# Optimization experiments

Measured on AMD Instinct MI355X. Metric: run time of the kernel, lower is better.

Reference implementation:

```python
import jax, jax.numpy as jnp
import numpy as np

B, T, C, H = 4, 2048, 1024, 16
HD = C // H  # head dim = 64


def setup_inputs() -> dict:
    key = jax.random.key(0)
    ks = jax.random.split(key, 5)
    s = 1.0 / np.sqrt(C)
    return {
        "x": jax.random.normal(ks[0], (B, T, C), jnp.float32),
        "Wk": jax.random.normal(ks[1], (C, C), jnp.float32) * s,
        "bk": jnp.zeros((C,), jnp.float32),
        "Wq": jax.random.normal(ks[2], (C, C), jnp.float32) * s,
        "bq": jnp.zeros((C,), jnp.float32),
        "Wv": jax.random.normal(ks[3], (C, C), jnp.float32) * s,
        "bv": jnp.zeros((C,), jnp.float32),
        "Wp": jax.random.normal(ks[4], (C, C), jnp.float32) * s,
        "bp": jnp.zeros((C,), jnp.float32),
    }


def reference(x, Wk, bk, Wq, bq, Wv, bv, Wp, bp):
    # Linear(in, out): y = x @ W.T + b  (W stored as [out, in], torch convention)
    k = (x @ Wk.T + bk).reshape(B, T, H, HD).transpose(0, 2, 1, 3)  # [B,H,T,HD]
    q = (x @ Wq.T + bq).reshape(B, T, H, HD).transpose(0, 2, 1, 3)
    v = (x @ Wv.T + bv).reshape(B, T, H, HD).transpose(0, 2, 1, 3)
    scale = 1.0 / np.sqrt(HD)
    att = jnp.einsum("bhqd,bhkd->bhqk", q, k) * scale  # [B,H,T,T]
    causal = jnp.tril(jnp.ones((T, T), bool))
    att = jnp.where(causal[None, None, :, :], att, -jnp.inf)
    att = jax.nn.softmax(att, axis=-1)
    y = jnp.einsum("bhqk,bhkd->bhqd", att, v)  # [B,H,T,HD]
    y = y.transpose(0, 2, 1, 3).reshape(B, T, C)
    return y @ Wp.T + bp
```

## Files before the change

kernel.cpp:

```cpp
#include <hip/hip_runtime.h>
#include <hip/hip_bf16.h>
#include <cmath>

#define Tt 2048
#define Cc 1024
#define Hh 16
#define HDd 64

typedef __attribute__((ext_vector_type(8))) short short8;
typedef __attribute__((ext_vector_type(4))) float f32x4;
typedef __attribute__((ext_vector_type(16))) float f32x16;

#define ASYNC16(gp, lp)                                       \
    __builtin_amdgcn_global_load_lds(                         \
        (const __attribute__((address_space(1))) void*)(gp),  \
        (__attribute__((address_space(3))) void*)(lp), 16, 0, 0)

__device__ __forceinline__ unsigned short f32_bf16(float f) {
    unsigned u = __float_as_uint(f);
    u += 0x7FFF + ((u >> 16) & 1);
    return (unsigned short)(u >> 16);
}
__device__ __forceinline__ unsigned short f32_bf16_rn(float f) {
    return (unsigned short)((__float_as_uint(f) + 0x8000u) >> 16);
}
__device__ __forceinline__ float fast_exp2(float x) {
#if __has_builtin(__builtin_amdgcn_exp2f)
    return __builtin_amdgcn_exp2f(x);
#else
    return exp2f(x);
#endif
}

__global__ __launch_bounds__(256) void cvt_all(
    const float* __restrict__ x, const float* __restrict__ a,
    const float* __restrict__ b, const float* __restrict__ c,
    const float* __restrict__ d, unsigned short* __restrict__ ox,
    unsigned short* __restrict__ oa, unsigned short* __restrict__ ob,
    unsigned short* __restrict__ oc, unsigned short* __restrict__ od) {
    const int id = blockIdx.x * 256 + threadIdx.x;
    const float* src; unsigned short* dst; int sub;
    if (id < 2097152) {
        src = x; dst = ox; sub = id;
    } else {
        const int wi = id - 2097152;
        const int which = wi >> 18;
        sub = wi & 262143;
        if (which == 0)      { src = a; dst = oa; }
        else if (which == 1) { src = b; dst = ob; }
        else if (which == 2) { src = c; dst = oc; }
        else                 { src = d; dst = od; }
    }
    float4 v = ((const float4*)src)[sub];
    ushort4 o;
    o.x = f32_bf16(v.x); o.y = f32_bf16(v.y);
    o.z = f32_bf16(v.z); o.w = f32_bf16(v.w);
    ((ushort4*)dst)[sub] = o;
}

__global__ __launch_bounds__(512, 2) void gemm_qkv8(
    const unsigned short* __restrict__ A,
    const unsigned short* __restrict__ Wcat,
    const float* __restrict__ bq, const float* __restrict__ bk,
    const float* __restrict__ bv,
    unsigned short* __restrict__ qout, unsigned short* __restrict__ kout,
    unsigned short* __restrict__ vout) {
    extern __shared__ unsigned short lds[];

    const int tid  = threadIdx.x;
    const int wid  = tid >> 6;
    const int lane = tid & 63;
    const int quad = lane >> 4;
    const int lr   = lane & 15;
    const int wr   = wid >> 2;
    const int wc   = wid & 3;

    const int id   = blockIdx.y * 8 + blockIdx.x;
    const int xcd  = id & 7;
    const int rank = id >> 3;
    const int by   = xcd * 4 + (rank >> 3);
    const int bx   = rank & 7;
    const int bm0  = by * 256;
    const int bn0  = bx * 256;

    const int srow  = wid * 8 + (lane >> 3);
    const int scol  = ((lane & 7) ^ (lane >> 3)) * 8;
    const int sldso = wid * 512;

    const int a_r   = wr * 64 + lr;
    const int b_r   = wc * 32 + lr;
    const int slot0 = (quad ^ (lr & 7)) * 8;
    const int slot1 = ((quad ^ 4) ^ (lr & 7)) * 8;

    f32x4 acc[8][4];
    const f32x4 zero = {0.f, 0.f, 0.f, 0.f};
#pragma unroll
    for (int i = 0; i < 8; ++i)
#pragma unroll
        for (int j = 0; j < 4; ++j) acc[i][j] = zero;

    short8 areg[4][2];
    short8 breg[2][2][2];

#define STG(S, BUF, REG, GB, GROW)                                          \
    do {                                                                    \
        if ((S) < 16) {                                                     \
            unsigned short* lb = lds + ((BUF) * 4 + (REG)) * 8192 + sldso;  \
            const unsigned short* gp =                                      \
                (GB) + (size_t)((GROW) + srow) * Cc + (S) * 64 + scol;      \
            ASYNC16(gp, lb);                                                \
            ASYNC16(gp + (size_t)64 * Cc, lb + 4096);                       \
        }                                                                   \
    } while (0)

#define LDA(mh)                                                             \
    do {                                                                    \
        const unsigned short* ab = bufb + (mh) * 8192;                      \
        _Pragma("unroll") for (int mf = 0; mf < 4; ++mf) {                  \
            areg[mf][0] = *(const short8*)(ab + (a_r + mf * 16) * 64 + slot0); \
            areg[mf][1] = *(const short8*)(ab + (a_r + mf * 16) * 64 + slot1); \
        }                                                                   \
    } while (0)

#define LDB(nh)                                                             \
    do {                                                                    \
        const unsigned short* bb = bufb + (2 + (nh)) * 8192;                \
        _Pragma("unroll") for (int nf = 0; nf < 2; ++nf) {                  \
            breg[nh][nf][0] = *(const short8*)(bb + (b_r + nf * 16) * 64 + slot0); \
            breg[nh][nf][1] = *(const short8*)(bb + (b_r + nf * 16) * 64 + slot1); \
        }                                                                   \
    } while (0)

#define MFMA_PHASE(mh, nh)                                                  \
    _Pragma("unroll") for (int mf = 0; mf < 4; ++mf)                        \
    _Pragma("unroll") for (int nf = 0; nf < 2; ++nf) {                      \
        acc[(mh)*4+mf][(nh)*2+nf] = __builtin_amdgcn_mfma_f32_16x16x32_bf16( \
            areg[mf][0], breg[nh][nf][0], acc[(mh)*4+mf][(nh)*2+nf], 0,0,0); \
        acc[(mh)*4+mf][(nh)*2+nf] = __builtin_amdgcn_mfma_f32_16x16x32_bf16( \
            areg[mf][1], breg[nh][nf][1], acc[(mh)*4+mf][(nh)*2+nf], 0,0,0); \
    }

#define TILE(T, BC, WN)                                                     \
    {                                                                       \
        const unsigned short* bufb = lds + (BC) * 32768;                    \
        LDA(0);                                                             \
        LDB(0);                                                             \
        STG((T) + 1, (BC) ^ 1, 1, A, bm0 + 128);                            \
        __builtin_amdgcn_s_barrier();                                       \
        asm volatile("s_waitcnt lgkmcnt(0)" ::: "memory");                  \
        __builtin_amdgcn_s_setprio(1);                                      \
        MFMA_PHASE(0, 0);                                                   \
        __builtin_amdgcn_s_setprio(0);                                      \
        __builtin_amdgcn_s_barrier();                                       \
        LDB(1);                                                             \
        STG((T) + 1, (BC) ^ 1, 3, Wcat, bn0 + 128);                         \
        __builtin_amdgcn_s_barrier();                                       \
        asm volatile("s_waitcnt lgkmcnt(0)" ::: "memory");                  \
        __builtin_amdgcn_s_setprio(1);                                      \
        MFMA_PHASE(0, 1);                                                   \
        __builtin_amdgcn_s_setprio(0);                                      \
        __builtin_amdgcn_s_barrier();                                       \
        LDA(1);                                                             \
        STG((T) + 2, (BC), 0, A, bm0);                                      \
        __builtin_amdgcn_s_barrier();                                       \
        asm volatile("s_waitcnt lgkmcnt(0)" ::: "memory");                  \
        __builtin_amdgcn_s_setprio(1);                                      \
        MFMA_PHASE(1, 0);                                                   \
        __builtin_amdgcn_s_setprio(0);                                      \
        __builtin_amdgcn_s_barrier();                                       \
        STG((T) + 2, (BC), 2, Wcat, bn0);                                   \
        __builtin_amdgcn_s_barrier();                                       \
        __builtin_amdgcn_s_setprio(1);                                      \
        MFMA_PHASE(1, 1);                                                   \
        __builtin_amdgcn_s_setprio(0);                                      \
        asm volatile("s_waitcnt vmcnt(" #WN ")" ::: "memory");              \
        __builtin_amdgcn_s_barrier();                                       \
    }

    STG(0, 0, 0, A, bm0);
    STG(0, 0, 1, A, bm0 + 128);
    STG(0, 0, 2, Wcat, bn0);
    STG(0, 0, 3, Wcat, bn0 + 128);
    STG(1, 1, 0, A, bm0);
    STG(1, 1, 2, Wcat, bn0);
    asm volatile("s_waitcnt vmcnt(4)" ::: "memory");
    __builtin_amdgcn_s_barrier();

    for (int t2 = 0; t2 < 7; ++t2) {
        const int T0 = t2 * 2;
        TILE(T0, 0, 4);
        TILE(T0 + 1, 1, 4);
    }
    TILE(14, 0, 0);
    TILE(15, 1, 0);

#undef TILE
#undef MFMA_PHASE
#undef LDB
#undef LDA
#undef STG

    const int which = bn0 >> 10;
    const float* bias = (which == 0) ? bq : bk;
    unsigned short* outp = (which == 0) ? qout : kout;
    const float scale = (which == 0) ? 0.1803368801111204f : 1.0f;
    const int nb = bn0 & 1023;
    (void)bv; (void)vout;

#pragma unroll
    for (int nh = 0; nh < 2; ++nh)
#pragma unroll
        for (int nf = 0; nf < 2; ++nf) {
            const int nl = nb + nh * 128 + wc * 32 + nf * 16 + lr;
            const float bvv = bias[nl];
            const int h = nl >> 6, hd = nl & 63;
#pragma unroll
            for (int mh = 0; mh < 2; ++mh)
#pragma unroll
                for (int mf = 0; mf < 4; ++mf) {
                    const f32x4 a = acc[mh * 4 + mf][nh * 2 + nf];
                    const int m0 = bm0 + mh * 128 + wr * 64 + mf * 16 + quad * 4;
                    const int b = m0 >> 11, t0 = m0 & 2047;
#pragma unroll
                    for (int r = 0; r < 4; ++r) {
                        outp[(((size_t)(b * Hh + h)) * Tt + t0 + r) * HDd + hd] =
                            f32_bf16_rn((a[r] + bvv) * scale);
                    }
                }
        }
}

__global__ __launch_bounds__(512, 2) void gemm_v8(
    const unsigned short* __restrict__ A,
    const unsigned short* __restrict__ Wcat,
    const float* __restrict__ bv,
    unsigned short* __restrict__ vout) {
    extern __shared__ unsigned short lds[];

    const int tid  = threadIdx.x;
    const int wid  = tid >> 6;
    const int lane = tid & 63;
    const int quad = lane >> 4;
    const int lr   = lane & 15;
    const int wr   = wid >> 2;
    const int wc   = wid & 3;

    const int id   = blockIdx.y * 8 + blockIdx.x;
    const int xcd  = id & 7;
    const int rank = id >> 3;
    const int by   = xcd * 4 + (rank >> 3);
    const int bx   = rank & 7;
    const int bm0  = by * 256;
    const int wrow0 = 2048 + bx * 128;

    const int srow  = wid * 8 + (lane >> 3);
    const int scol  = ((lane & 7) ^ (lane >> 3)) * 8;
    const int sldso = wid * 512;

    const int a_r   = wr * 64 + lr;
    const int b_r2  = (wc & 1) * 32 + lr;
    const int breg_off = 16384 + (wc >> 1) * 4096;
    const int slot0 = (quad ^ (lr & 7)) * 8;
    const int slot1 = ((quad ^ 4) ^ (lr & 7)) * 8;

    f32x4 acc[8][2];
    const f32x4 zero = {0.f, 0.f, 0.f, 0.f};
#pragma unroll
    for (int i = 0; i < 8; ++i)
#pragma unroll
        for (int j = 0; j < 2; ++j) acc[i][j] = zero;

    short8 areg[4][2];
    short8 breg[2][2];

#define STGAV(S, BUF, REG_OFF, GROW)                                        \
    do {                                                                    \
        if ((S) < 16) {                                                     \
            unsigned short* lb = lds + (BUF) * 24576 + (REG_OFF) + sldso;   \
            const unsigned short* gp =                                      \
                A + (size_t)(bm0 + (GROW) + srow) * Cc + (S) * 64 + scol;   \
            ASYNC16(gp, lb);                                                \
            ASYNC16(gp + (size_t)64 * Cc, lb + 4096);                       \
        }                                                                   \
    } while (0)

#define STGBV(S, BUF, REG_OFF, NROW)                                        \
    do {                                                                    \
        if ((S) < 16) {                                                     \
            unsigned short* lb = lds + (BUF) * 24576 + (REG_OFF) + sldso;   \
            const unsigned short* gp =                                      \
                Wcat + (size_t)(wrow0 + (NROW) + srow) * Cc + (S) * 64 + scol; \
            ASYNC16(gp, lb);                                                \
        }                                                                   \
    } while (0)

#define LDA_V(mh)                                                           \
    do {                                                                    \
        const unsigned short* ab = bufb + (mh) * 8192;                      \
        _Pragma("unroll") for (int mf = 0; mf < 4; ++mf) {                  \
            areg[mf][0] = *(const short8*)(ab + (a_r + mf * 16) * 64 + slot0); \
            areg[mf][1] = *(const short8*)(ab + (a_r + mf * 16) * 64 + slot1); \
        }                                                                   \
    } while (0)

#define LDB_V                                                               \
    do {                                                                    \
        const unsigned short* bb = bufb + breg_off;                         \
        _Pragma("unroll") for (int nf = 0; nf < 2; ++nf) {                  \
            breg[nf][0] = *(const short8*)(bb + (b_r2 + nf * 16) * 64 + slot0); \
            breg[nf][1] = *(const short8*)(bb + (b_r2 + nf * 16) * 64 + slot1); \
        }                                                                   \
    } while (0)

#define MFMA_V(mh)                                                          \
    _Pragma("unroll") for (int mf = 0; mf < 4; ++mf)                        \
    _Pragma("unroll") for (int nf = 0; nf < 2; ++nf) {                      \
        acc[(mh)*4+mf][nf] = __builtin_amdgcn_mfma_f32_16x16x32_bf16(       \
            areg[mf][0], breg[nf][0], acc[(mh)*4+mf][nf], 0, 0, 0);         \
        acc[(mh)*4+mf][nf] = __builtin_amdgcn_mfma_f32_16x16x32_bf16(       \
            areg[mf][1], breg[nf][1], acc[(mh)*4+mf][nf], 0, 0, 0);         \
    }

#define TILE_V(T, BC, WN)                                                   \
    {                                                                       \
        const unsigned short* bufb = lds + (BC) * 24576;                    \
        LDA_V(0);                                                           \
        LDB_V;                                                              \
        STGAV((T) + 1, (BC) ^ 1, 8192, 128);                                \
        STGBV((T) + 1, (BC) ^ 1, 20480, 64);                                \
        __builtin_amdgcn_s_barrier();                                       \
        asm volatile("s_waitcnt lgkmcnt(0)" ::: "memory");                  \
        __builtin_amdgcn_s_setprio(1);                                      \
        MFMA_V(0);                                                          \
        __builtin_amdgcn_s_setprio(0);                                      \
        __builtin_amdgcn_s_barrier();                                       \
        LDA_V(1);                                                           \
        STGAV((T) + 2, (BC), 0, 0);                                         \
        STGBV((T) + 2, (BC), 16384, 0);                                     \
        __builtin_amdgcn_s_barrier();                                       \
        asm volatile("s_waitcnt lgkmcnt(0)" ::: "memory");                  \
        __builtin_amdgcn_s_setprio(1);                                      \
        MFMA_V(1);                                                          \
        __builtin_amdgcn_s_setprio(0);                                      \
        asm volatile("s_waitcnt vmcnt(" #WN ")" ::: "memory");              \
        __builtin_amdgcn_s_barrier();                                       \
    }

    STGAV(0, 0, 0, 0);
    STGAV(0, 0, 8192, 128);
    STGBV(0, 0, 16384, 0);
    STGBV(0, 0, 20480, 64);
    STGAV(1, 1, 0, 0);
    STGBV(1, 1, 16384, 0);
    asm volatile("s_waitcnt vmcnt(3)" ::: "memory");
    __builtin_amdgcn_s_barrier();

    for (int t2 = 0; t2 < 7; ++t2) {
        const int T0 = t2 * 2;
        TILE_V(T0, 0, 3);
        TILE_V(T0 + 1, 1, 3);
    }
    TILE_V(14, 0, 0);
    TILE_V(15, 1, 0);

#undef TILE_V
#undef MFMA_V
#undef LDB_V
#undef LDA_V
#undef STGBV
#undef STGAV

#pragma unroll
    for (int nf = 0; nf < 2; ++nf) {
        const int nl = (wrow0 - 2048) + wc * 32 + nf * 16 + lr;
        const float bvv = bv[nl];
        const int h = nl >> 6, hd = nl & 63;
#pragma unroll
        for (int mh = 0; mh < 2; ++mh)
#pragma unroll
            for (int mf = 0; mf < 4; ++mf) {
                const f32x4 a = acc[mh * 4 + mf][nf];
                const int m0 = bm0 + mh * 128 + wr * 64 + mf * 16 + quad * 4;
                const int b = m0 >> 11, t0 = m0 & 2047;
                ushort4 pk;
                pk.x = f32_bf16_rn(a[0] + bvv);
                pk.y = f32_bf16_rn(a[1] + bvv);
                pk.z = f32_bf16_rn(a[2] + bvv);
                pk.w = f32_bf16_rn(a[3] + bvv);
                *(ushort4*)(vout + (((size_t)(b * Hh + h)) * HDd + hd) * Tt + t0) = pk;
            }
    }
}

__global__ __launch_bounds__(512, 2) void gemm_proj8(
    const unsigned short* __restrict__ A,
    const unsigned short* __restrict__ W,
    const float* __restrict__ bias,
    float* __restrict__ out) {
    extern __shared__ unsigned short lds[];

    const int tid  = threadIdx.x;
    const int wid  = tid >> 6;
    const int lane = tid & 63;
    const int quad = lane >> 4;
    const int lr   = lane & 15;
    const int wr   = wid >> 2;
    const int wc   = wid & 3;

    const int id   = blockIdx.y * 8 + blockIdx.x;
    const int xcd  = id & 7;
    const int rank = id >> 3;
    const int by   = xcd * 4 + (rank >> 3);
    const int bx   = rank & 7;
    const int bm0  = by * 256;
    const int bn0  = bx * 128;

    const int srow  = wid * 8 + (lane >> 3);
    const int scol  = ((lane & 7) ^ (lane >> 3)) * 8;
    const int sldso = wid * 512;

    const int a_r   = wr * 64 + lr;
    const int b_r2  = (wc & 1) * 32 + lr;
    const int breg_off = 16384 + (wc >> 1) * 4096;
    const int slot0 = (quad ^ (lr & 7)) * 8;
    const int slot1 = ((quad ^ 4) ^ (lr & 7)) * 8;

    f32x4 acc[8][2];
    const f32x4 zero = {0.f, 0.f, 0.f, 0.f};
#pragma unroll
    for (int i = 0; i < 8; ++i)
#pragma unroll
        for (int j = 0; j < 2; ++j) acc[i][j] = zero;

    short8 areg[4][2];
    short8 breg[2][2];

#define STGA(S, BUF, REG_OFF, GROW)                                         \
    do {                                                                    \
        if ((S) < 16) {                                                     \
            unsigned short* lb = lds + (BUF) * 24576 + (REG_OFF) + sldso;   \
            const unsigned short* gp =                                      \
                A + (size_t)(bm0 + (GROW) + srow) * Cc + (S) * 64 + scol;   \
            ASYNC16(gp, lb);                                                \
            ASYNC16(gp + (size_t)64 * Cc, lb + 4096);                       \
        }                                                                   \
    } while (0)

#define STGB(S, BUF, REG_OFF, NROW)                                         \
    do {                                                                    \
        if ((S) < 16) {                                                     \
            unsigned short* lb = lds + (BUF) * 24576 + (REG_OFF) + sldso;   \
            const unsigned short* gp =                                      \
                W + (size_t)(bn0 + (NROW) + srow) * Cc + (S) * 64 + scol;   \
            ASYNC16(gp, lb);                                                \
        }                                                                   \
    } while (0)

#define LDA_P(mh)                                                           \
    do {                                                                    \
        const unsigned short* ab = bufb + (mh) * 8192;                      \
        _Pragma("unroll") for (int mf = 0; mf < 4; ++mf) {                  \
            areg[mf][0] = *(const short8*)(ab + (a_r + mf * 16) * 64 + slot0); \
            areg[mf][1] = *(const short8*)(ab + (a_r + mf * 16) * 64 + slot1); \
        }                                                                   \
    } while (0)

#define LDB_P                                                               \
    do {                                                                    \
        const unsigned short* bb = bufb + breg_off;                         \
        _Pragma("unroll") for (int nf = 0; nf < 2; ++nf) {                  \
            breg[nf][0] = *(const short8*)(bb + (b_r2 + nf * 16) * 64 + slot0); \
            breg[nf][1] = *(const short8*)(bb + (b_r2 + nf * 16) * 64 + slot1); \
        }                                                                   \
    } while (0)

#define MFMA_P(mh)                                                          \
    _Pragma("unroll") for (int mf = 0; mf < 4; ++mf)                        \
    _Pragma("unroll") for (int nf = 0; nf < 2; ++nf) {                      \
        acc[(mh)*4+mf][nf] = __builtin_amdgcn_mfma_f32_16x16x32_bf16(       \
            areg[mf][0], breg[nf][0], acc[(mh)*4+mf][nf], 0, 0, 0);         \
        acc[(mh)*4+mf][nf] = __builtin_amdgcn_mfma_f32_16x16x32_bf16(       \
            areg[mf][1], breg[nf][1], acc[(mh)*4+mf][nf], 0, 0, 0);         \
    }

#define TILE_P(T, BC, WN)                                                   \
    {                                                                       \
        const unsigned short* bufb = lds + (BC) * 24576;                    \
        LDA_P(0);                                                           \
        LDB_P;                                                              \
        STGA((T) + 1, (BC) ^ 1, 8192, 128);                                 \
        STGB((T) + 1, (BC) ^ 1, 20480, 64);                                 \
        __builtin_amdgcn_s_barrier();                                       \
        asm volatile("s_waitcnt lgkmcnt(0)" ::: "memory");                  \
        __builtin_amdgcn_s_setprio(1);                                      \
        MFMA_P(0);                                                          \
        __builtin_amdgcn_s_setprio(0);                                      \
        __builtin_amdgcn_s_barrier();                                       \
        LDA_P(1);                                                           \
        STGA((T) + 2, (BC), 0, 0);                                          \
        STGB((T) + 2, (BC), 16384, 0);                                      \
        __builtin_amdgcn_s_barrier();                                       \
        asm volatile("s_waitcnt lgkmcnt(0)" ::: "memory");                  \
        __builtin_amdgcn_s_setprio(1);                                      \
        MFMA_P(1);                                                          \
        __builtin_amdgcn_s_setprio(0);                                      \
        asm volatile("s_waitcnt vmcnt(" #WN ")" ::: "memory");              \
        __builtin_amdgcn_s_barrier();                                       \
    }

    STGA(0, 0, 0, 0);
    STGA(0, 0, 8192, 128);
    STGB(0, 0, 16384, 0);
    STGB(0, 0, 20480, 64);
    STGA(1, 1, 0, 0);
    STGB(1, 1, 16384, 0);
    asm volatile("s_waitcnt vmcnt(3)" ::: "memory");
    __builtin_amdgcn_s_barrier();

    for (int t2 = 0; t2 < 7; ++t2) {
        const int T0 = t2 * 2;
        TILE_P(T0, 0, 3);
        TILE_P(T0 + 1, 1, 3);
    }
    TILE_P(14, 0, 0);
    TILE_P(15, 1, 0);

#undef TILE_P
#undef MFMA_P
#undef LDB_P
#undef LDA_P
#undef STGB
#undef STGA

#pragma unroll
    for (int nf = 0; nf < 2; ++nf) {
        const int n = bn0 + wc * 32 + nf * 16 + lr;
        const float bvv = bias[n];
#pragma unroll
        for (int mh = 0; mh < 2; ++mh)
#pragma unroll
            for (int mf = 0; mf < 4; ++mf) {
                const f32x4 a = acc[mh * 4 + mf][nf];
                const int m0 = bm0 + mh * 128 + wr * 64 + mf * 16 + quad * 4;
#pragma unroll
                for (int r = 0; r < 4; ++r)
                    out[(size_t)(m0 + r) * Cc + n] = a[r] + bvv;
            }
    }
}

__global__ __launch_bounds__(256, 2) void attn(const unsigned short* __restrict__ q,
                                               const unsigned short* __restrict__ k,
                                               const unsigned short* __restrict__ vt,
                                               unsigned short* __restrict__ y) {
    __shared__ unsigned short sK[2][64 * 64];
    __shared__ unsigned short sV[2][64 * 64];

    const int tid  = threadIdx.x;
    const int wid  = tid >> 6;
    const int lane = tid & 63;
    const int l31  = lane & 31;
    const int hb   = lane >> 5;
    const int x7   = lane & 7;

    const int bh = blockIdx.x;
    const int qx = blockIdx.y;
    const size_t headq = (size_t)bh * Tt * HDd;
    const unsigned short* kg = k + headq;
    const unsigned short* vg = vt + headq;
    const int b = bh >> 4, h = bh & 15;

    const int g_r = lane >> 3;
    const int g_c = ((lane & 7) ^ g_r) * 8;
    const unsigned short* kst = kg + (size_t)(wid * 16 + g_r) * HDd + g_c;
    const unsigned short* vst = vg + (size_t)(wid * 16 + g_r) * Tt + g_c;
    unsigned short* dK0 = sK[0] + wid * 1024;
    unsigned short* dK1 = sK[1] + wid * 1024;
    unsigned short* dV0 = sV[0] + wid * 1024;
    unsigned short* dV1 = sV[1] + wid * 1024;

#define STAGE_KV(BUF, KB)                                                   \
    do {                                                                    \
        unsigned short* dK = (BUF) ? dK1 : dK0;                             \
        unsigned short* dV = (BUF) ? dV1 : dV0;                             \
        ASYNC16(kst + (size_t)(KB) * HDd,       dK);                        \
        ASYNC16(kst + (size_t)((KB) + 8) * HDd, dK + 512);                  \
        ASYNC16(vst + (KB),                     dV);                        \
        ASYNC16(vst + (size_t)8 * Tt + (KB),    dV + 512);                  \
    } while (0)

#define CVTPK(d, a, bb) asm("v_cvt_pk_bf16_f32 %0, %1, %2" : "=v"(d) : "v"(a), "v"(bb))
#define PLSWAP(xx, yy)  asm("v_permlane32_swap_b32 %0, %1" : "+v"(xx), "+v"(yy))

    const int frow = l31 * 64;

    const f32x16 zero16 = {0.f,0.f,0.f,0.f,0.f,0.f,0.f,0.f,
                           0.f,0.f,0.f,0.f,0.f,0.f,0.f,0.f};

    const int nwoff = 1 + (wid >> 1);

    for (int pass = 0; pass < 2; ++pass) {
        const int qt = pass ? (15 - qx) : qx;
        const int qb = qt * 128;
        const int ntiles = 2 * qt + 2;
        const int nw = 2 * qt + nwoff;

        const unsigned short* qp =
            q + headq + (size_t)(qb + wid * 32 + l31) * HDd;
        short8 qf[4];
#pragma unroll
        for (int c = 0; c < 4; c++)
            qf[c] = *(const short8*)(qp + c * 16 + hb * 8);

        f32x16 o0 = zero16, o1 = zero16;
        float l_run = 0.f;

        STAGE_KV(0, 0);
        __syncthreads();

        for (int kt = 0; kt < ntiles; ++kt) {
            const int cur = kt & 1;
            if (kt + 1 < ntiles) STAGE_KV(cur ^ 1, (kt + 1) * 64);

            if (kt < nw) {
                const unsigned short* bK = sK[cur];
                const unsigned short* bV = sV[cur];

                f32x16 p0 = zero16, p1 = zero16;
                __builtin_amdgcn_s_setprio(1);
#pragma unroll
                for (int c = 0; c < 4; c++) {
                    const int cs = ((2 * c + hb) ^ x7) * 8;
                    short8 kf0 = *(const short8*)(bK + frow + cs);
                    short8 kf1 = *(const short8*)(bK + 2048 + frow + cs);
                    p0 = __builtin_amdgcn_mfma_f32_32x32x16_bf16(kf0, qf[c], p0, 0, 0, 0);
                    p1 = __builtin_amdgcn_mfma_f32_32x32x16_bf16(kf1, qf[c], p1, 0, 0, 0);
                }
                __builtin_amdgcn_s_setprio(0);

                if (kt == nw - 1 || kt == ntiles - 1) {
                    const int qd = qb + wid * 32 + l31 - kt * 64 - 4 * hb;
#pragma unroll
                    for (int r = 0; r < 16; r++) {
                        const int kb0 = (r & 3) + 8 * (r >> 2);
                        p0[r] = (kb0 <= qd) ? p0[r] : -INFINITY;
                        p1[r] = (kb0 + 32 <= qd) ? p1[r] : -INFINITY;
                    }
                }

                float lacc = 0.f;
#pragma unroll
                for (int r = 0; r < 16; r++) {
                    p0[r] = fast_exp2(p0[r]); lacc += p0[r];
                    p1[r] = fast_exp2(p1[r]); lacc += p1[r];
                }
                l_run += lacc;

                unsigned w0[4][2], w1[4][2];
#pragma unroll
                for (int g = 0; g < 4; g++) {
                    CVTPK(w0[g][0], p0[4 * g + 0], p0[4 * g + 1]);
                    CVTPK(w0[g][1], p0[4 * g + 2], p0[4 * g + 3]);
                    CVTPK(w1[g][0], p1[4 * g + 0], p1[4 * g + 1]);
                    CVTPK(w1[g][1], p1[4 * g + 2], p1[4 * g + 3]);
                }

                __builtin_amdgcn_s_setprio(1);
#pragma unroll
                for (int kc = 0; kc < 4; kc++) {
                    unsigned x0, x1, y0, y1;
                    if (kc == 0)      { x0 = w0[0][0]; x1 = w0[0][1]; y0 = w0[1][0]; y1 = w0[1][1]; }
                    else if (kc == 1) { x0 = w0[2][0]; x1 = w0[2][1]; y0 = w0[3][0]; y1 = w0[3][1]; }
                    else if (kc == 2) { x0 = w1[0][0]; x1 = w1[0][1]; y0 = w1[1][0]; y1 = w1[1][1]; }
                    else              { x0 = w1[2][0]; x1 = w1[2][1]; y0 = w1[3][0]; y1 = w1[3][1]; }
                    PLSWAP(x0, y0);
                    PLSWAP(x1, y1);
                    union { unsigned u[4]; short8 s; } pu;
                    pu.u[0] = x0; pu.u[1] = x1; pu.u[2] = y0; pu.u[3] = y1;

                    const int vs = ((2 * kc + hb) ^ x7) * 8;
                    short8 vf0 = *(const short8*)(bV + frow + vs);
                    short8 vf1 = *(const short8*)(bV + 2048 + frow + vs);
                    o0 = __builtin_amdgcn_mfma_f32_32x32x16_bf16(pu.s, vf0, o0, 0, 0, 0);
                    o1 = __builtin_amdgcn_mfma_f32_32x32x16_bf16(pu.s, vf1, o1, 0, 0, 0);
                }
                __builtin_amdgcn_s_setprio(0);
            }

            __syncthreads();
        }

        l_run += __shfl_xor(l_run, 32);
        const float inv = 1.0f / l_run;
        unsigned short* yp = y + (size_t)(b * Tt + qb + wid * 32) * Cc + h * HDd;
#pragma unroll
        for (int r = 0; r < 16; r++) {
            const int qr = (r & 3) + 8 * (r >> 2) + 4 * hb;
            const float invr = __shfl(inv, qr);
            yp[(size_t)qr * Cc + l31]      = f32_bf16_rn(o0[r] * invr);
            yp[(size_t)qr * Cc + 32 + l31] = f32_bf16_rn(o1[r] * invr);
        }
    }
#undef STAGE_KV
#undef CVTPK
#undef PLSWAP
}

extern "C" void kernel_launch(void* const* d_in, const int* in_sizes, int n_in,
                              void* d_out, int out_size, void* d_ws, size_t ws_size,
                              hipStream_t stream) {
    const float* x  = (const float*)d_in[0];
    const float* Wk = (const float*)d_in[1];
    const float* bk = (const float*)d_in[2];
    const float* Wq = (const float*)d_in[3];
    const float* bq = (const float*)d_in[4];
    const float* Wv = (const float*)d_in[5];
    const float* bv = (const float*)d_in[6];
    const float* Wp = (const float*)d_in[7];
    const float* bp = (const float*)d_in[8];
    float* out = (float*)d_out;

    char* ws = (char*)d_ws;
    size_t off = 0;
    auto alloc = [&](size_t bytes) { char* p = ws + off; off += bytes; return p; };
    const size_t MK = (size_t)8192 * 1024;
    const size_t NK = (size_t)1024 * 1024;
    unsigned short* xb   = (unsigned short*)alloc(MK * 2);
    unsigned short* Wcat = (unsigned short*)alloc(3 * NK * 2);
    unsigned short* Wqb  = Wcat;
    unsigned short* Wkb  = Wcat + NK;
    unsigned short* Wvb  = Wcat + 2 * NK;
    unsigned short* Wpb  = (unsigned short*)alloc(NK * 2);
    unsigned short* qh   = (unsigned short*)alloc(MK * 2);
    unsigned short* kh   = (unsigned short*)alloc(MK * 2);
    unsigned short* vth  = (unsigned short*)alloc(MK * 2);
    unsigned short* ya   = (unsigned short*)alloc(MK * 2);

    static bool lds_attr_set = false;
    if (!lds_attr_set) {
        (void)hipFuncSetAttribute((const void*)gemm_qkv8,
                                  hipFuncAttributeMaxDynamicSharedMemorySize,
                                  131072);
        (void)hipFuncSetAttribute((const void*)gemm_v8,
                                  hipFuncAttributeMaxDynamicSharedMemorySize,
                                  98304);
        (void)hipFuncSetAttribute((const void*)gemm_proj8,
                                  hipFuncAttributeMaxDynamicSharedMemorySize,
                                  98304);
        lds_attr_set = true;
    }

    cvt_all<<<12288, 256, 0, stream>>>(x, Wq, Wk, Wv, Wp, xb, Wqb, Wkb, Wvb, Wpb);

    gemm_qkv8<<<dim3(8, 32), 512, 131072, stream>>>(xb, Wcat, bq, bk, bv, qh, kh, vth);
    gemm_v8<<<dim3(8, 32), 512, 98304, stream>>>(xb, Wcat, bv, vth);

    attn<<<dim3(64, 8), 256, 0, stream>>>(qh, kh, vth, ya);

    gemm_proj8<<<dim3(8, 32), 512, 98304, stream>>>(ya, Wpb, bp, out);
}
```

Measured before the change: 229.2 us.

## Merge QK and V GEMMs into one launch and split attention into per-tile blocks

The separate QK and V projection kernels become one launch with 512 blocks that branch on block index, so one launch is saved and the two GEMMs can overlap. The attention kernel no longer loops over a paired short/long query tile in two passes. Each block now handles a single query tile from a 16-wide grid with a reordered tile mapping, and launch bounds are raised to 4 blocks per CU. This should improve occupancy and load balance but loses the explicit pairing, and the V part now reserves the larger 128 KB LDS allocation.

```diff
diff --git a/kernel.cpp b/kernel.cpp
--- a/kernel.cpp
+++ b/kernel.cpp
@@ -58,15 +58,12 @@
     ((ushort4*)dst)[sub] = o;
 }
 
-__global__ __launch_bounds__(512, 2) void gemm_qkv8(
+__device__ __forceinline__ void qk_body(
+    unsigned short* lds, const int id,
     const unsigned short* __restrict__ A,
     const unsigned short* __restrict__ Wcat,
     const float* __restrict__ bq, const float* __restrict__ bk,
-    const float* __restrict__ bv,
-    unsigned short* __restrict__ qout, unsigned short* __restrict__ kout,
-    unsigned short* __restrict__ vout) {
-    extern __shared__ unsigned short lds[];
-
+    unsigned short* __restrict__ qout, unsigned short* __restrict__ kout) {
     const int tid  = threadIdx.x;
     const int wid  = tid >> 6;
     const int lane = tid & 63;
@@ -75,7 +72,6 @@
     const int wr   = wid >> 2;
     const int wc   = wid & 3;
 
-    const int id   = blockIdx.y * 8 + blockIdx.x;
     const int xcd  = id & 7;
     const int rank = id >> 3;
     const int by   = xcd * 4 + (rank >> 3);
@@ -205,7 +201,6 @@
     unsigned short* outp = (which == 0) ? qout : kout;
     const float scale = (which == 0) ? 0.1803368801111204f : 1.0f;
     const int nb = bn0 & 1023;
-    (void)bv; (void)vout;
 
 #pragma unroll
     for (int nh = 0; nh < 2; ++nh)
@@ -230,13 +225,12 @@
         }
 }
 
-__global__ __launch_bounds__(512, 2) void gemm_v8(
+__device__ __forceinline__ void v_body(
+    unsigned short* lds, const int id,
     const unsigned short* __restrict__ A,
     const unsigned short* __restrict__ Wcat,
     const float* __restrict__ bv,
     unsigned short* __restrict__ vout) {
-    extern __shared__ unsigned short lds[];
-
     const int tid  = threadIdx.x;
     const int wid  = tid >> 6;
     const int lane = tid & 63;
@@ -245,7 +239,6 @@
     const int wr   = wid >> 2;
     const int wc   = wid & 3;
 
-    const int id   = blockIdx.y * 8 + blockIdx.x;
     const int xcd  = id & 7;
     const int rank = id >> 3;
     const int by   = xcd * 4 + (rank >> 3);
@@ -392,6 +385,21 @@
     }
 }
 
+__global__ __launch_bounds__(512, 2) void gemm_fused(
+    const unsigned short* __restrict__ A,
+    const unsigned short* __restrict__ Wcat,
+    const float* __restrict__ bq, const float* __restrict__ bk,
+    const float* __restrict__ bv,
+    unsigned short* __restrict__ qout, unsigned short* __restrict__ kout,
+    unsigned short* __restrict__ vout) {
+    extern __shared__ unsigned short lds[];
+    const int id = blockIdx.y * 8 + blockIdx.x;
+    if (id < 256)
+        qk_body(lds, id, A, Wcat, bq, bk, qout, kout);
+    else
+        v_body(lds, id - 256, A, Wcat, bv, vout);
+}
+
 __global__ __launch_bounds__(512, 2) void gemm_proj8(
     const unsigned short* __restrict__ A,
     const unsigned short* __restrict__ W,
@@ -549,7 +557,7 @@
     }
 }
 
-__global__ __launch_bounds__(256, 2) void attn(const unsigned short* __restrict__ q,
+__global__ __launch_bounds__(256, 4) void attn(const unsigned short* __restrict__ q,
                                                const unsigned short* __restrict__ k,
                                                const unsigned short* __restrict__ vt,
                                                unsigned short* __restrict__ y) {
@@ -564,7 +572,8 @@
     const int x7   = lane & 7;
 
     const int bh = blockIdx.x;
-    const int qx = blockIdx.y;
+    const int yb = blockIdx.y;
+    const int qt = (yb & 4) ? ((yb & 8) ? yb - 12 : yb + 4) : 15 - yb;
     const size_t headq = (size_t)bh * Tt * HDd;
     const unsigned short* kg = k + headq;
     const unsigned short* vg = vt + headq;
@@ -597,109 +606,104 @@
     const f32x16 zero16 = {0.f,0.f,0.f,0.f,0.f,0.f,0.f,0.f,
                            0.f,0.f,0.f,0.f,0.f,0.f,0.f,0.f};
 
-    const int nwoff = 1 + (wid >> 1);
-
-    for (int pass = 0; pass < 2; ++pass) {
-        const int qt = pass ? (15 - qx) : qx;
-        const int qb = qt * 128;
-        const int ntiles = 2 * qt + 2;
-        const int nw = 2 * qt + nwoff;
-
-        const unsigned short* qp =
-            q + headq + (size_t)(qb + wid * 32 + l31) * HDd;
-        short8 qf[4];
-#pragma unroll
-        for (int c = 0; c < 4; c++)
-            qf[c] = *(const short8*)(qp + c * 16 + hb * 8);
-
-        f32x16 o0 = zero16, o1 = zero16;
-        float l_run = 0.f;
-
-        STAGE_KV(0, 0);
+    const int qb = qt * 128;
+    const int ntiles = 2 * qt + 2;
+    const int nw = 2 * qt + 1 + (wid >> 1);
+
+    const unsigned short* qp =
+        q + headq + (size_t)(qb + wid * 32 + l31) * HDd;
+    short8 qf[4];
+#pragma unroll
+    for (int c = 0; c < 4; c++)
+        qf[c] = *(const short8*)(qp + c * 16 + hb * 8);
+
+    f32x16 o0 = zero16, o1 = zero16;
+    float l_run = 0.f;
+
+    STAGE_KV(0, 0);
+    __syncthreads();
+
+    for (int kt = 0; kt < ntiles; ++kt) {
+        const int cur = kt & 1;
+        if (kt + 1 < ntiles) STAGE_KV(cur ^ 1, (kt + 1) * 64);
+
+        if (kt < nw) {
+            const unsigned short* bK = sK[cur];
+            const unsigned short* bV = sV[cur];
+
+            f32x16 p0 = zero16, p1 = zero16;
+            __builtin_amdgcn_s_setprio(1);
+#pragma unroll
+            for (int c = 0; c < 4; c++) {
+                const int cs = ((2 * c + hb) ^ x7) * 8;
+                short8 kf0 = *(const short8*)(bK + frow + cs);
+                short8 kf1 = *(const short8*)(bK + 2048 + frow + cs);
+                p0 = __builtin_amdgcn_mfma_f32_32x32x16_bf16(kf0, qf[c], p0, 0, 0, 0);
+                p1 = __builtin_amdgcn_mfma_f32_32x32x16_bf16(kf1, qf[c], p1, 0, 0, 0);
+            }
+            __builtin_amdgcn_s_setprio(0);
+
+            if (kt == nw - 1 || kt == ntiles - 1) {
+                const int qd = qb + wid * 32 + l31 - kt * 64 - 4 * hb;
+#pragma unroll
+                for (int r = 0; r < 16; r++) {
+                    const int kb0 = (r & 3) + 8 * (r >> 2);
+                    p0[r] = (kb0 <= qd) ? p0[r] : -INFINITY;
+                    p1[r] = (kb0 + 32 <= qd) ? p1[r] : -INFINITY;
+                }
+            }
+
+            float lacc = 0.f;
+#pragma unroll
+            for (int r = 0; r < 16; r++) {
+                p0[r] = fast_exp2(p0[r]); lacc += p0[r];
+                p1[r] = fast_exp2(p1[r]); lacc += p1[r];
+            }
+            l_run += lacc;
+
+            unsigned w0[4][2], w1[4][2];
+#pragma unroll
+            for (int g = 0; g < 4; g++) {
+                CVTPK(w0[g][0], p0[4 * g + 0], p0[4 * g + 1]);
+                CVTPK(w0[g][1], p0[4 * g + 2], p0[4 * g + 3]);
+                CVTPK(w1[g][0], p1[4 * g + 0], p1[4 * g + 1]);
+                CVTPK(w1[g][1], p1[4 * g + 2], p1[4 * g + 3]);
+            }
+
+            __builtin_amdgcn_s_setprio(1);
+#pragma unroll
+            for (int kc = 0; kc < 4; kc++) {
+                unsigned x0, x1, y0, y1;
+                if (kc == 0)      { x0 = w0[0][0]; x1 = w0[0][1]; y0 = w0[1][0]; y1 = w0[1][1]; }
+                else if (kc == 1) { x0 = w0[2][0]; x1 = w0[2][1]; y0 = w0[3][0]; y1 = w0[3][1]; }
+                else if (kc == 2) { x0 = w1[0][0]; x1 = w1[0][1]; y0 = w1[1][0]; y1 = w1[1][1]; }
+                else              { x0 = w1[2][0]; x1 = w1[2][1]; y0 = w1[3][0]; y1 = w1[3][1]; }
+                PLSWAP(x0, y0);
+                PLSWAP(x1, y1);
+                union { unsigned u[4]; short8 s; } pu;
+                pu.u[0] = x0; pu.u[1] = x1; pu.u[2] = y0; pu.u[3] = y1;
+
+                const int vs = ((2 * kc + hb) ^ x7) * 8;
+                short8 vf0 = *(const short8*)(bV + frow + vs);
+                short8 vf1 = *(const short8*)(bV + 2048 + frow + vs);
+                o0 = __builtin_amdgcn_mfma_f32_32x32x16_bf16(pu.s, vf0, o0, 0, 0, 0);
+                o1 = __builtin_amdgcn_mfma_f32_32x32x16_bf16(pu.s, vf1, o1, 0, 0, 0);
+            }
+            __builtin_amdgcn_s_setprio(0);
+        }
+
         __syncthreads();
-
-        for (int kt = 0; kt < ntiles; ++kt) {
-            const int cur = kt & 1;
-            if (kt + 1 < ntiles) STAGE_KV(cur ^ 1, (kt + 1) * 64);
-
-            if (kt < nw) {
-                const unsigned short* bK = sK[cur];
-                const unsigned short* bV = sV[cur];
-
-                f32x16 p0 = zero16, p1 = zero16;
-                __builtin_amdgcn_s_setprio(1);
-#pragma unroll
-                for (int c = 0; c < 4; c++) {
-                    const int cs = ((2 * c + hb) ^ x7) * 8;
-                    short8 kf0 = *(const short8*)(bK + frow + cs);
-                    short8 kf1 = *(const short8*)(bK + 2048 + frow + cs);
-                    p0 = __builtin_amdgcn_mfma_f32_32x32x16_bf16(kf0, qf[c], p0, 0, 0, 0);
-                    p1 = __builtin_amdgcn_mfma_f32_32x32x16_bf16(kf1, qf[c], p1, 0, 0, 0);
-                }
-                __builtin_amdgcn_s_setprio(0);
-
-                if (kt == nw - 1 || kt == ntiles - 1) {
-                    const int qd = qb + wid * 32 + l31 - kt * 64 - 4 * hb;
-#pragma unroll
-                    for (int r = 0; r < 16; r++) {
-                        const int kb0 = (r & 3) + 8 * (r >> 2);
-                        p0[r] = (kb0 <= qd) ? p0[r] : -INFINITY;
-                        p1[r] = (kb0 + 32 <= qd) ? p1[r] : -INFINITY;
-                    }
-                }
-
-                float lacc = 0.f;
-#pragma unroll
-                for (int r = 0; r < 16; r++) {
-                    p0[r] = fast_exp2(p0[r]); lacc += p0[r];
-                    p1[r] = fast_exp2(p1[r]); lacc += p1[r];
-                }
-                l_run += lacc;
-
-                unsigned w0[4][2], w1[4][2];
-#pragma unroll
-                for (int g = 0; g < 4; g++) {
-                    CVTPK(w0[g][0], p0[4 * g + 0], p0[4 * g + 1]);
-                    CVTPK(w0[g][1], p0[4 * g + 2], p0[4 * g + 3]);
-                    CVTPK(w1[g][0], p1[4 * g + 0], p1[4 * g + 1]);
-                    CVTPK(w1[g][1], p1[4 * g + 2], p1[4 * g + 3]);
-                }
-
-                __builtin_amdgcn_s_setprio(1);
-#pragma unroll
-                for (int kc = 0; kc < 4; kc++) {
-                    unsigned x0, x1, y0, y1;
-                    if (kc == 0)      { x0 = w0[0][0]; x1 = w0[0][1]; y0 = w0[1][0]; y1 = w0[1][1]; }
-                    else if (kc == 1) { x0 = w0[2][0]; x1 = w0[2][1]; y0 = w0[3][0]; y1 = w0[3][1]; }
-                    else if (kc == 2) { x0 = w1[0][0]; x1 = w1[0][1]; y0 = w1[1][0]; y1 = w1[1][1]; }
-                    else              { x0 = w1[2][0]; x1 = w1[2][1]; y0 = w1[3][0]; y1 = w1[3][1]; }
-                    PLSWAP(x0, y0);
-                    PLSWAP(x1, y1);
-                    union { unsigned u[4]; short8 s; } pu;
-                    pu.u[0] = x0; pu.u[1] = x1; pu.u[2] = y0; pu.u[3] = y1;
-
-                    const int vs = ((2 * kc + hb) ^ x7) * 8;
-                    short8 vf0 = *(const short8*)(bV + frow + vs);
-                    short8 vf1 = *(const short8*)(bV + 2048 + frow + vs);
-                    o0 = __builtin_amdgcn_mfma_f32_32x32x16_bf16(pu.s, vf0, o0, 0, 0, 0);
-                    o1 = __builtin_amdgcn_mfma_f32_32x32x16_bf16(pu.s, vf1, o1, 0, 0, 0);
-                }
-                __builtin_amdgcn_s_setprio(0);
-            }
-
-            __syncthreads();
-        }
-
-        l_run += __shfl_xor(l_run, 32);
-        const float inv = 1.0f / l_run;
-        unsigned short* yp = y + (size_t)(b * Tt + qb + wid * 32) * Cc + h * HDd;
-#pragma unroll
-        for (int r = 0; r < 16; r++) {
-            const int qr = (r & 3) + 8 * (r >> 2) + 4 * hb;
-            const float invr = __shfl(inv, qr);
-            yp[(size_t)qr * Cc + l31]      = f32_bf16_rn(o0[r] * invr);
-            yp[(size_t)qr * Cc + 32 + l31] = f32_bf16_rn(o1[r] * invr);
-        }
+    }
+
+    l_run += __shfl_xor(l_run, 32);
+    const float inv = 1.0f / l_run;
+    unsigned short* yp = y + (size_t)(b * Tt + qb + wid * 32) * Cc + h * HDd;
+#pragma unroll
+    for (int r = 0; r < 16; r++) {
+        const int qr = (r & 3) + 8 * (r >> 2) + 4 * hb;
+        const float invr = __shfl(inv, qr);
+        yp[(size_t)qr * Cc + l31]      = f32_bf16_rn(o0[r] * invr);
+        yp[(size_t)qr * Cc + 32 + l31] = f32_bf16_rn(o1[r] * invr);
     }
 #undef STAGE_KV
 #undef CVTPK
@@ -738,12 +742,9 @@
 
     static bool lds_attr_set = false;
     if (!lds_attr_set) {
-        (void)hipFuncSetAttribute((const void*)gemm_qkv8,
+        (void)hipFuncSetAttribute((const void*)gemm_fused,
                                   hipFuncAttributeMaxDynamicSharedMemorySize,
                                   131072);
-        (void)hipFuncSetAttribute((const void*)gemm_v8,
-                                  hipFuncAttributeMaxDynamicSharedMemorySize,
-                                  98304);
         (void)hipFuncSetAttribute((const void*)gemm_proj8,
                                   hipFuncAttributeMaxDynamicSharedMemorySize,
                                   98304);
@@ -752,10 +753,9 @@
 
     cvt_all<<<12288, 256, 0, stream>>>(x, Wq, Wk, Wv, Wp, xb, Wqb, Wkb, Wvb, Wpb);
 
-    gemm_qkv8<<<dim3(8, 32), 512, 131072, stream>>>(xb, Wcat, bq, bk, bv, qh, kh, vth);
-    gemm_v8<<<dim3(8, 32), 512, 98304, stream>>>(xb, Wcat, bv, vth);
-
-    attn<<<dim3(64, 8), 256, 0, stream>>>(qh, kh, vth, ya);
+    gemm_fused<<<dim3(8, 64), 512, 131072, stream>>>(xb, Wcat, bq, bk, bv, qh, kh, vth);
+
+    attn<<<dim3(64, 16), 256, 0, stream>>>(qh, kh, vth, ya);
 
     gemm_proj8<<<dim3(8, 32), 512, 98304, stream>>>(ya, Wpb, bp, out);
 }
```

After: 231.9 us. About the same (+1.2%).
